# Kernel optimization log

Hardware: AMD Instinct MI355X
Metric: run time of the kernel (lower is better)

## Reference

```python
import jax, jax.numpy as jnp
import numpy as np

N = 200000
D = 128
MAX_DEG = 12
BN_EPS = 1e-5


def setup_inputs() -> dict:
    key = jax.random.key(0)
    ks = jax.random.split(key, 8)
    s = 0.1
    feat = jax.random.normal(ks[0], (N, D), dtype=jnp.float32)
    W_ih = jax.random.normal(ks[1], (3 * D, D), dtype=jnp.float32) * s
    W_hh = jax.random.normal(ks[2], (3 * D, D), dtype=jnp.float32) * s
    b_ih = jax.random.normal(ks[3], (3 * D,), dtype=jnp.float32) * s
    b_hh = jax.random.normal(ks[4], (3 * D,), dtype=jnp.float32) * s
    W_self = jax.random.normal(ks[5], (D, D), dtype=jnp.float32) * s
    W_neigh = jax.random.normal(ks[6], (D, D), dtype=jnp.float32) * s
    gamma = jnp.ones((D,), dtype=jnp.float32)
    beta = jnp.zeros((D,), dtype=jnp.float32)
    # Ragged per-node mailboxes: random in-degree in [0, MAX_DEG], padded.
    rng = np.random.default_rng(0)
    deg = rng.integers(0, MAX_DEG + 1, size=N)
    src_idx = rng.integers(0, N, size=(N, MAX_DEG)).astype(np.int32)
    mask = (np.arange(MAX_DEG)[None, :] < deg[:, None])
    return {
        'feat': feat, 'gamma': gamma, 'beta': beta,
        'W_ih': W_ih, 'W_hh': W_hh, 'b_ih': b_ih, 'b_hh': b_hh,
        'W_self': W_self, 'W_neigh': W_neigh,
        'src_idx': jnp.asarray(src_idx), 'mask': jnp.asarray(mask),
    }


def _eopa_forward(feat, gamma, beta, W_ih, W_hh, b_ih, b_hh, W_self, W_neigh, src_idx, mask):
    # BatchNorm1d (training mode: batch statistics, biased variance)
    mu = jnp.mean(feat, axis=0)
    var = jnp.mean((feat - mu) ** 2, axis=0)
    x = (feat - mu) * jax.lax.rsqrt(var + BN_EPS) * gamma + beta  # [N, D]

    # Precompute input-gate projections are gathered per-step; scan over mailbox slots.
    def step(h, inp):
        src_t, m_t = inp            # [N] int, [N] bool
        xt = x[src_t]               # gather neighbor messages  [N, D]
        gi = xt @ W_ih.T + b_ih     # [N, 3D]
        gh = h @ W_hh.T + b_hh      # [N, 3D]
        ir, iz, inn = jnp.split(gi, 3, axis=1)
        hr, hz, hn = jnp.split(gh, 3, axis=1)
        r = jax.nn.sigmoid(ir + hr)
        z = jax.nn.sigmoid(iz + hz)
        n = jnp.tanh(inn + r * hn)
        h_new = (1.0 - z) * n + z * h
        # freeze hidden state past each node's true in-degree (ragged GRU)
        h = jnp.where(m_t[:, None], h_new, h)
        return h, None

    h0 = jnp.zeros_like(x)
    neigh, _ = jax.lax.scan(step, h0, (src_idx.T, mask.T))  # scan over MAX_DEG steps
    rst = x @ W_self.T + neigh @ W_neigh.T
    return rst


def reference(feat, gamma, beta, W_ih, W_hh, b_ih, b_hh, W_self, W_neigh, src_idx, mask):
    return _eopa_forward(feat, gamma, beta, W_ih, W_hh, b_ih, b_hh, W_self, W_neigh, src_idx, mask)
```

## Files before the change

kernel.cpp:

```cpp
#include <hip/hip_runtime.h>
#include <hip/hip_bf16.h>
#include <stdint.h>

#define NN 200000
#define DD 128

typedef __attribute__((ext_vector_type(8))) short short8;
typedef __attribute__((ext_vector_type(4))) float floatx4;

#define MFMA16(a,b,c) __builtin_amdgcn_mfma_f32_16x16x32_bf16(a,b,c,0,0,0)

static constexpr size_t WS_SUM    = 0;
static constexpr size_t WS_SQ     = 4096;
static constexpr size_t WS_FLAG   = 8192;
static constexpr size_t WS_HIST   = 8256;
static constexpr size_t WS_OFF    = 8384;
static constexpr size_t WS_WHH    = 16384;
static constexpr size_t WS_WIH    = 114688;
static constexpr size_t WS_WSELF  = 212992;
static constexpr size_t WS_WNEIGH = 245760;
static constexpr size_t WS_DEG    = 278528;
static constexpr size_t WS_PERM   = 478528;
static constexpr size_t WS_XB     = 1278528;

__device__ __forceinline__ uint16_t f2b(float f){
    uint32_t u = __builtin_bit_cast(uint32_t, f);
    uint32_t r = u + 0x7FFFu + ((u >> 16) & 1u);
    return (uint16_t)(r >> 16);
}
__device__ __forceinline__ float b2f(uint16_t h){
    uint32_t u = ((uint32_t)h) << 16;
    return __builtin_bit_cast(float, u);
}
__device__ __forceinline__ float sigm(float x){
    float e = __builtin_amdgcn_exp2f(x * -1.4426950408889634f);
    return __builtin_amdgcn_rcpf(1.0f + e);
}
__device__ __forceinline__ float tanh_(float x){
    float e = __builtin_amdgcn_exp2f(x * 2.8853900817779268f);
    return 1.0f - 2.0f * __builtin_amdgcn_rcpf(1.0f + e);
}

__global__ void k_init(float* __restrict__ ws){
#pragma unroll
    for (int k = 0; k < 9; k++) ws[threadIdx.x + k * 256] = 0.0f;
}

__global__ void k_detect(const uint32_t* __restrict__ mask_w, uint32_t* __restrict__ flag){
    __shared__ uint32_t any;
    if (threadIdx.x == 0) any = 0;
    __syncthreads();
    uint32_t loc = 0;
    for (int i = threadIdx.x; i < 4096; i += 256) loc |= (mask_w[i] & 0xFFFFFF00u);
    if (loc) atomicOr(&any, 1u);
    __syncthreads();
    if (threadIdx.x == 0) *flag = (any != 0) ? 1u : 0u;
}

__global__ void k_stats(const float* __restrict__ feat, float* __restrict__ wsum, float* __restrict__ wsq){
    __shared__ float rs_[256][5], rq_[256][5];
    const int cg = threadIdx.x & 31, rr = threadIdx.x >> 5;
    float s0=0,s1=0,s2=0,s3=0,q0=0,q1=0,q2=0,q3=0;
    const float4* f4 = (const float4*)feat;
    for (int r = blockIdx.x * 8 + rr; r < NN; r += gridDim.x * 8){
        float4 v = f4[(size_t)r * 32 + cg];
        s0+=v.x; s1+=v.y; s2+=v.z; s3+=v.w;
        q0+=v.x*v.x; q1+=v.y*v.y; q2+=v.z*v.z; q3+=v.w*v.w;
    }
    rs_[threadIdx.x][0]=s0; rs_[threadIdx.x][1]=s1; rs_[threadIdx.x][2]=s2; rs_[threadIdx.x][3]=s3;
    rq_[threadIdx.x][0]=q0; rq_[threadIdx.x][1]=q1; rq_[threadIdx.x][2]=q2; rq_[threadIdx.x][3]=q3;
    __syncthreads();
    if (threadIdx.x < 32){
        const int rep = (blockIdx.x & 7) * 128;
#pragma unroll
        for (int k = 0; k < 4; k++){
            float a = 0.f, b = 0.f;
#pragma unroll
            for (int r = 0; r < 8; r++){ a += rs_[r*32+threadIdx.x][k]; b += rq_[r*32+threadIdx.x][k]; }
            atomicAdd(&wsum[rep + threadIdx.x*4 + k], a);
            atomicAdd(&wsq [rep + threadIdx.x*4 + k], b);
        }
    }
}

__global__ void k_prep(const float* __restrict__ Wih, const float* __restrict__ Whh,
                       const float* __restrict__ Wself, const float* __restrict__ Wneigh,
                       uint16_t* __restrict__ whh_c, uint16_t* __restrict__ wih_c,
                       uint16_t* __restrict__ wself_c, uint16_t* __restrict__ wneigh_c){
    int i = blockIdx.x * 256 + threadIdx.x;
    if (i < 49152){
        int j = i & 7, cidx = i >> 3, n = cidx % 384, kq = cidx / 384;
        whh_c[i] = f2b(Whh[n * 128 + kq * 8 + j]);
    } else if (i < 98304){
        int e = i - 49152;
        int j = e & 7, cidx = e >> 3, n = cidx % 384, kq = cidx / 384;
        wih_c[e] = f2b(Wih[n * 128 + kq * 8 + j]);
    } else if (i < 114688){
        int e = i - 98304;
        int j = e & 7, cidx = e >> 3, n = cidx & 127, kq = cidx >> 7;
        wself_c[e] = f2b(Wself[n * 128 + kq * 8 + j]);
    } else {
        int e = i - 114688;
        int j = e & 7, cidx = e >> 3, n = cidx & 127, kq = cidx >> 7;
        wneigh_c[e] = f2b(Wneigh[n * 128 + kq * 8 + j]);
    }
}

__global__ void k_hist(const void* __restrict__ mask, const uint32_t* __restrict__ flag,
                       uint8_t* __restrict__ deg, uint32_t* __restrict__ hist){
    __shared__ uint32_t lh[13];
    if (threadIdx.x < 13) lh[threadIdx.x] = 0;
    __syncthreads();
    const uint32_t flg = *flag;
    for (int n = blockIdx.x * 256 + threadIdx.x; n < NN; n += gridDim.x * 256){
        int d = 0;
        if (flg){
            const uint8_t* m = (const uint8_t*)mask + (size_t)n * 12;
            for (int t = 0; t < 12; t++) d += m[t] ? 1 : 0;
        } else {
            const int* m = (const int*)mask + (size_t)n * 12;
            for (int t = 0; t < 12; t++) d += m[t] ? 1 : 0;
        }
        deg[n] = (uint8_t)d;
        atomicAdd(&lh[d], 1u);
    }
    __syncthreads();
    if (threadIdx.x < 13 && lh[threadIdx.x]) atomicAdd(&hist[threadIdx.x], lh[threadIdx.x]);
}

__global__ void k_scan(const uint32_t* __restrict__ hist, uint32_t* __restrict__ off){
    if (threadIdx.x == 0){
        uint32_t acc = 0;
        for (int d = 12; d >= 0; d--){ off[d] = acc; acc += hist[d]; }
    }
}

__global__ void k_scatter(const uint8_t* __restrict__ deg, uint32_t* __restrict__ off,
                          int* __restrict__ perm){
    __shared__ uint32_t lh[13], basebuf[13];
    if (threadIdx.x < 13) lh[threadIdx.x] = 0;
    __syncthreads();
    int n = blockIdx.x * 256 + threadIdx.x;
    int d = 0; uint32_t r = 0;
    bool valid = n < NN;
    if (valid){ d = deg[n]; r = atomicAdd(&lh[d], 1u); }
    __syncthreads();
    if (threadIdx.x < 13 && lh[threadIdx.x]) basebuf[threadIdx.x] = atomicAdd(&off[threadIdx.x], lh[threadIdx.x]);
    __syncthreads();
    if (valid) perm[basebuf[d] + r] = n;
}

__global__ void k_bn(const float* __restrict__ feat, const float* __restrict__ gamma,
                     const float* __restrict__ beta, const float* __restrict__ wsum,
                     const float* __restrict__ wsq, uint16_t* __restrict__ xb){
    const int c8 = (threadIdx.x & 15) * 8;
    const int rr = threadIdx.x >> 4;
    float g[8], b[8];
#pragma unroll
    for (int k = 0; k < 8; k++){
        int col = c8 + k;
        float su = 0.f, sq = 0.f;
#pragma unroll
        for (int r = 0; r < 8; r++){ su += wsum[r*128+col]; sq += wsq[r*128+col]; }
        float mu  = su * (1.0f / NN);
        float var = sq * (1.0f / NN) - mu * mu;
        float rs  = rsqrtf(var + 1e-5f);
        float gg  = gamma[col] * rs;
        g[k] = gg; b[k] = beta[col] - mu * gg;
    }
    for (int r = blockIdx.x * 16 + rr; r < NN; r += gridDim.x * 16){
        const float4* f4 = (const float4*)(feat + (size_t)r * 128 + c8);
        float4 v0 = f4[0], v1 = f4[1];
        short8 o;
        o[0]=(short)f2b(v0.x*g[0]+b[0]); o[1]=(short)f2b(v0.y*g[1]+b[1]);
        o[2]=(short)f2b(v0.z*g[2]+b[2]); o[3]=(short)f2b(v0.w*g[3]+b[3]);
        o[4]=(short)f2b(v1.x*g[4]+b[4]); o[5]=(short)f2b(v1.y*g[5]+b[5]);
        o[6]=(short)f2b(v1.z*g[6]+b[6]); o[7]=(short)f2b(v1.w*g[7]+b[7]);
        *(short8*)(xb + (size_t)r * 128 + c8) = o;
    }
}

__global__ __launch_bounds__(512, 2) void k_gru(
    const uint16_t* __restrict__ xb,
    const uint16_t* __restrict__ whh_c, const uint16_t* __restrict__ wih_c,
    const uint16_t* __restrict__ wself_c, const uint16_t* __restrict__ wneigh_c,
    const float* __restrict__ b_ih, const float* __restrict__ b_hh,
    const int* __restrict__ src_idx, const void* __restrict__ mask,
    const uint32_t* __restrict__ flag, const int* __restrict__ perm,
    const uint8_t* __restrict__ degp, float* __restrict__ out)
{
    __shared__ __align__(16) uint16_t hbuf[2][64][136];
    __shared__ int src_s[768];
    __shared__ uint8_t mask_s[768];
    __shared__ int perm_s[64];
    __shared__ int tmax_s;

    const int tid = threadIdx.x, lane = tid & 63, w = tid >> 6, q = lane >> 4, c = lane & 15;
    const int base = blockIdx.x * 64;

    if (tid < 64) perm_s[tid] = perm[base + tid];
    if (tid == 0) tmax_s = 0;
    __syncthreads();

    const uint32_t flg = *flag;
    for (int i = tid; i < 768; i += 512){
        int node = perm_s[i / 12];
        size_t offn = (size_t)node * 12 + (i % 12);
        src_s[i] = src_idx[offn];
        uint8_t mv;
        if (flg) mv = ((const uint8_t*)mask)[offn] ? 1 : 0;
        else     mv = ((const int*)mask)[offn] ? 1 : 0;
        mask_s[i] = mv;
    }
    if (tid < 64) atomicMax(&tmax_s, (int)degp[perm_s[tid]]);
    for (int i = tid; i < 64 * 136 * 2 / 4; i += 512) ((uint32_t*)hbuf[0])[i] = 0;

    short8 Bi[3][4], Bh[3][4];
    float bs0, bs1, bi2, bh2;
    {
        const int n0 = w * 16 + c;
#pragma unroll
        for (int g = 0; g < 3; g++){
            int n = g * 128 + n0;
#pragma unroll
            for (int kb = 0; kb < 4; kb++){
                Bi[g][kb] = *(const short8*)(wih_c + ((size_t)(kb * 4 + q) * 384 + n) * 8);
                Bh[g][kb] = *(const short8*)(whh_c + ((size_t)(kb * 4 + q) * 384 + n) * 8);
            }
        }
        bs0 = b_ih[n0]       + b_hh[n0];
        bs1 = b_ih[128 + n0] + b_hh[128 + n0];
        bi2 = b_ih[256 + n0];
        bh2 = b_hh[256 + n0];
    }

    float hC[4][4];
#pragma unroll
    for (int m = 0; m < 4; m++)
#pragma unroll
        for (int j = 0; j < 4; j++) hC[m][j] = 0.f;

    __syncthreads();
    const int tmax = tmax_s;

    if (tmax > 0){
        short8 Ax[4][4];
#pragma unroll
        for (int m = 0; m < 4; m++){
            int s = src_s[(m * 16 + c) * 12];
            const uint16_t* a = xb + (size_t)s * 128 + q * 8;
#pragma unroll
            for (int kb = 0; kb < 4; kb++) Ax[m][kb] = *(const short8*)(a + kb * 32);
        }
        for (int t = 0; t < tmax; t++){
            const int rb = t & 1, wbuf = rb ^ 1;
            const int tn = (t + 1 < tmax) ? t + 1 : t;
#pragma unroll
            for (int m = 0; m < 4; m++){
                short8 Ah[4];
#pragma unroll
                for (int kb = 0; kb < 4; kb++)
                    Ah[kb] = *(const short8*)&hbuf[rb][m * 16 + c][kb * 32 + q * 8];
                floatx4 agi[3], agh[3];
#pragma unroll
                for (int g = 0; g < 3; g++){
                    floatx4 x0 = {0.f, 0.f, 0.f, 0.f}, h0 = {0.f, 0.f, 0.f, 0.f};
#pragma unroll
                    for (int kb = 0; kb < 4; kb++){
                        x0 = MFMA16(Ax[m][kb], Bi[g][kb], x0);
                        h0 = MFMA16(Ah[kb],    Bh[g][kb], h0);
                    }
                    agi[g] = x0; agh[g] = h0;
                }
                {
                    int s = src_s[(m * 16 + c) * 12 + tn];
                    const uint16_t* a = xb + (size_t)s * 128 + q * 8;
#pragma unroll
                    for (int kb = 0; kb < 4; kb++) Ax[m][kb] = *(const short8*)(a + kb * 32);
                }
#pragma unroll
                for (int j = 0; j < 4; j++){
                    uint8_t mk = mask_s[(m * 16 + q * 4 + j) * 12 + t];
                    float r  = sigm(agi[0][j] + agh[0][j] + bs0);
                    float z  = sigm(agi[1][j] + agh[1][j] + bs1);
                    float hn = agh[2][j] + bh2;
                    float nn = tanh_(agi[2][j] + bi2 + r * hn);
                    float hold = hC[m][j];
                    float hnew = nn + z * (hold - nn);
                    hnew = mk ? hnew : hold;
                    hC[m][j] = hnew;
                    hbuf[wbuf][m * 16 + q * 4 + j][w * 16 + c] = f2b(hnew);
                }
            }
            asm volatile("s_waitcnt lgkmcnt(0)\n\ts_barrier" ::: "memory");
        }
    }

    const int fb = tmax & 1;

    floatx4 acc2[4];
#pragma unroll
    for (int m = 0; m < 4; m++) acc2[m] = floatx4{0.f, 0.f, 0.f, 0.f};
    short8 Bs_[4], Bn_[4];
#pragma unroll
    for (int kb = 0; kb < 4; kb++){
        Bs_[kb] = *(const short8*)(wself_c  + ((size_t)(kb * 4 + q) * 128 + w * 16 + c) * 8);
        Bn_[kb] = *(const short8*)(wneigh_c + ((size_t)(kb * 4 + q) * 128 + w * 16 + c) * 8);
    }
#pragma unroll
    for (int m = 0; m < 4; m++){
        short8 A[4];
#pragma unroll
        for (int kb = 0; kb < 4; kb++)
            A[kb] = *(const short8*)&hbuf[fb][m * 16 + c][kb * 32 + q * 8];
#pragma unroll
        for (int kb = 0; kb < 4; kb++) acc2[m] = MFMA16(A[kb], Bn_[kb], acc2[m]);
        int xrow = perm_s[m * 16 + c];
        const uint16_t* a = xb + (size_t)xrow * 128 + q * 8;
#pragma unroll
        for (int kb = 0; kb < 4; kb++) A[kb] = *(const short8*)(a + kb * 32);
#pragma unroll
        for (int kb = 0; kb < 4; kb++) acc2[m] = MFMA16(A[kb], Bs_[kb], acc2[m]);
    }
#pragma unroll
    for (int m = 0; m < 4; m++){
#pragma unroll
        for (int j = 0; j < 4; j++){
            int orow = perm_s[m * 16 + q * 4 + j];
            out[(size_t)orow * 128 + w * 16 + c] = acc2[m][j];
        }
    }
}

extern "C" void kernel_launch(void* const* d_in, const int* in_sizes, int n_in,
                              void* d_out, int out_size, void* d_ws, size_t ws_size,
                              hipStream_t stream) {
    const float* feat    = (const float*)d_in[0];
    const float* gamma   = (const float*)d_in[1];
    const float* beta    = (const float*)d_in[2];
    const float* W_ih    = (const float*)d_in[3];
    const float* W_hh    = (const float*)d_in[4];
    const float* b_ih    = (const float*)d_in[5];
    const float* b_hh    = (const float*)d_in[6];
    const float* W_self  = (const float*)d_in[7];
    const float* W_neigh = (const float*)d_in[8];
    const int*   src_idx = (const int*)d_in[9];
    const void*  mask    = (const void*)d_in[10];
    float* out = (float*)d_out;

    char* ws = (char*)d_ws;
    float*    wsum     = (float*)(ws + WS_SUM);
    float*    wsq      = (float*)(ws + WS_SQ);
    uint32_t* flag     = (uint32_t*)(ws + WS_FLAG);
    uint32_t* hist     = (uint32_t*)(ws + WS_HIST);
    uint32_t* off      = (uint32_t*)(ws + WS_OFF);
    uint16_t* whh_c    = (uint16_t*)(ws + WS_WHH);
    uint16_t* wih_c    = (uint16_t*)(ws + WS_WIH);
    uint16_t* wself_c  = (uint16_t*)(ws + WS_WSELF);
    uint16_t* wneigh_c = (uint16_t*)(ws + WS_WNEIGH);
    uint8_t*  deg      = (uint8_t*)(ws + WS_DEG);
    int*      perm     = (int*)(ws + WS_PERM);
    uint16_t* xb       = (uint16_t*)(ws + WS_XB);

    k_init   <<<1,    256, 0, stream>>>((float*)ws);
    k_detect <<<1,    256, 0, stream>>>((const uint32_t*)mask, flag);
    k_stats  <<<512,  256, 0, stream>>>(feat, wsum, wsq);
    k_prep   <<<512,  256, 0, stream>>>(W_ih, W_hh, W_self, W_neigh, whh_c, wih_c, wself_c, wneigh_c);
    k_hist   <<<256,  256, 0, stream>>>(mask, flag, deg, hist);
    k_scan   <<<1,    64,  0, stream>>>(hist, off);
    k_scatter<<<782,  256, 0, stream>>>(deg, off, perm);
    k_bn     <<<782,  256, 0, stream>>>(feat, gamma, beta, wsum, wsq, xb);
    k_gru    <<<3125, 512, 0, stream>>>(xb, whh_c, wih_c, wself_c, wneigh_c, b_ih, b_hh,
                                        src_idx, mask, flag, perm, deg, out);
}
```

Measured before the change: 755.6 us.

## Split GRU block into producer waves for input gates and consumer waves for recurrence

Warps 0-3 now gather neighbor features and compute the input-gate projections (x·W_ih + b_ih) one step ahead, storing them as bf16 in a double-buffered shared-memory array. Warps 4-7 handle only the recurrent h·W_hh matmul and the gate math, running at raised wave priority. The aim is to take gather latency and half the MFMA work off the serial recurrence's critical path. In exchange it adds shared-memory traffic and capacity use, and it rounds the input gates to bf16, which slightly changes numerics.

```diff
diff --git a/kernel.cpp b/kernel.cpp
--- a/kernel.cpp
+++ b/kernel.cpp
@@ -7,8 +7,10 @@
 
 typedef __attribute__((ext_vector_type(8))) short short8;
 typedef __attribute__((ext_vector_type(4))) float floatx4;
+typedef __attribute__((ext_vector_type(2))) unsigned int uint32x2;
 
 #define MFMA16(a,b,c) __builtin_amdgcn_mfma_f32_16x16x32_bf16(a,b,c,0,0,0)
+#define LGKM_BARRIER() asm volatile("s_waitcnt lgkmcnt(0)\n\ts_barrier" ::: "memory")
 
 static constexpr size_t WS_SUM    = 0;
 static constexpr size_t WS_SQ     = 4096;
@@ -190,6 +192,7 @@
     const uint8_t* __restrict__ degp, float* __restrict__ out)
 {
     __shared__ __align__(16) uint16_t hbuf[2][64][136];
+    __shared__ __align__(16) uint16_t gis[2][4][24][64][4];
     __shared__ int src_s[768];
     __shared__ uint8_t mask_s[768];
     __shared__ int perm_s[64];
@@ -213,86 +216,121 @@
         mask_s[i] = mv;
     }
     if (tid < 64) atomicMax(&tmax_s, (int)degp[perm_s[tid]]);
-    for (int i = tid; i < 64 * 136 * 2 / 4; i += 512) ((uint32_t*)hbuf[0])[i] = 0;
-
-    short8 Bi[3][4], Bh[3][4];
-    float bs0, bs1, bi2, bh2;
+    for (int i = tid; i < 64 * 136 * 2 / 2; i += 512) ((uint32_t*)hbuf[0])[i] = 0;
+
+    const bool producer = (w < 4);
+    const int rw = producer ? w : (w - 4);
+
+    short8 Bf[6][4];
+    float bias6[6];
     {
-        const int n0 = w * 16 + c;
-#pragma unroll
-        for (int g = 0; g < 3; g++){
-            int n = g * 128 + n0;
-#pragma unroll
-            for (int kb = 0; kb < 4; kb++){
-                Bi[g][kb] = *(const short8*)(wih_c + ((size_t)(kb * 4 + q) * 384 + n) * 8);
-                Bh[g][kb] = *(const short8*)(whh_c + ((size_t)(kb * 4 + q) * 384 + n) * 8);
+        const uint16_t* wsrc = producer ? wih_c : whh_c;
+        const float*    bsrc = producer ? b_ih  : b_hh;
+#pragma unroll
+        for (int g = 0; g < 3; g++)
+#pragma unroll
+            for (int dg = 0; dg < 2; dg++){
+                const int gd = g * 2 + dg;
+                const int n = g * 128 + rw * 32 + dg * 16 + c;
+                bias6[gd] = bsrc[n];
+#pragma unroll
+                for (int kb = 0; kb < 4; kb++)
+                    Bf[gd][kb] = *(const short8*)(wsrc + ((size_t)(kb * 4 + q) * 384 + n) * 8);
             }
-        }
-        bs0 = b_ih[n0]       + b_hh[n0];
-        bs1 = b_ih[128 + n0] + b_hh[128 + n0];
-        bi2 = b_ih[256 + n0];
-        bh2 = b_hh[256 + n0];
-    }
-
-    float hC[4][4];
-#pragma unroll
-    for (int m = 0; m < 4; m++)
-#pragma unroll
-        for (int j = 0; j < 4; j++) hC[m][j] = 0.f;
+    }
 
     __syncthreads();
     const int tmax = tmax_s;
 
-    if (tmax > 0){
+    if (producer){
         short8 Ax[4][4];
-#pragma unroll
-        for (int m = 0; m < 4; m++){
-            int s = src_s[(m * 16 + c) * 12];
-            const uint16_t* a = xb + (size_t)s * 128 + q * 8;
-#pragma unroll
-            for (int kb = 0; kb < 4; kb++) Ax[m][kb] = *(const short8*)(a + kb * 32);
-        }
+        auto gatherAx = [&](int tg){
+#pragma unroll
+            for (int m = 0; m < 4; m++){
+                int s = src_s[(m * 16 + c) * 12 + tg];
+                const uint16_t* a = xb + (size_t)s * 128 + q * 8;
+#pragma unroll
+                for (int kb = 0; kb < 4; kb++) Ax[m][kb] = *(const short8*)(a + kb * 32);
+            }
+        };
+        auto giStep = [&](int slot){
+#pragma unroll
+            for (int m = 0; m < 4; m++){
+#pragma unroll
+                for (int gd = 0; gd < 6; gd++){
+                    floatx4 a0 = {0.f, 0.f, 0.f, 0.f};
+#pragma unroll
+                    for (int kb = 0; kb < 4; kb++) a0 = MFMA16(Ax[m][kb], Bf[gd][kb], a0);
+                    const float bb = bias6[gd];
+                    uint32x2 v;
+                    v[0] = ((uint32_t)f2b(a0[1] + bb) << 16) | f2b(a0[0] + bb);
+                    v[1] = ((uint32_t)f2b(a0[3] + bb) << 16) | f2b(a0[2] + bb);
+                    *(uint32x2*)&gis[slot][rw][gd * 4 + m][lane][0] = v;
+                }
+            }
+        };
+        if (tmax > 0){
+            gatherAx(0);
+            giStep(0);
+            gatherAx(tmax > 1 ? 1 : 0);
+        }
+        LGKM_BARRIER();
+        for (int t = 0; t < tmax; t++){
+            if (t + 1 < tmax){
+                giStep((t + 1) & 1);
+                gatherAx(t + 2 < tmax ? t + 2 : tmax - 1);
+            }
+            LGKM_BARRIER();
+        }
+    } else {
+        float hC[4][2][4] = {};
+        LGKM_BARRIER();
         for (int t = 0; t < tmax; t++){
             const int rb = t & 1, wbuf = rb ^ 1;
-            const int tn = (t + 1 < tmax) ? t + 1 : t;
+            __builtin_amdgcn_s_setprio(1);
 #pragma unroll
             for (int m = 0; m < 4; m++){
                 short8 Ah[4];
 #pragma unroll
                 for (int kb = 0; kb < 4; kb++)
                     Ah[kb] = *(const short8*)&hbuf[rb][m * 16 + c][kb * 32 + q * 8];
-                floatx4 agi[3], agh[3];
-#pragma unroll
-                for (int g = 0; g < 3; g++){
-                    floatx4 x0 = {0.f, 0.f, 0.f, 0.f}, h0 = {0.f, 0.f, 0.f, 0.f};
-#pragma unroll
-                    for (int kb = 0; kb < 4; kb++){
-                        x0 = MFMA16(Ax[m][kb], Bi[g][kb], x0);
-                        h0 = MFMA16(Ah[kb],    Bh[g][kb], h0);
+                floatx4 ac[6];
+#pragma unroll
+                for (int gd = 0; gd < 6; gd++){
+                    floatx4 a0 = {0.f, 0.f, 0.f, 0.f};
+#pragma unroll
+                    for (int kb = 0; kb < 4; kb++) a0 = MFMA16(Ah[kb], Bf[gd][kb], a0);
+                    ac[gd] = a0;
+                }
+                uint32x2 gp[6];
+#pragma unroll
+                for (int gd = 0; gd < 6; gd++)
+                    gp[gd] = *(const uint32x2*)&gis[rb][rw][gd * 4 + m][lane][0];
+                uint8_t mk[4];
+#pragma unroll
+                for (int j = 0; j < 4; j++) mk[j] = mask_s[(m * 16 + q * 4 + j) * 12 + t];
+#pragma unroll
+                for (int dg = 0; dg < 2; dg++){
+#pragma unroll
+                    for (int j = 0; j < 4; j++){
+                        uint32_t w0 = gp[dg][j >> 1], w1 = gp[2 + dg][j >> 1], w2 = gp[4 + dg][j >> 1];
+                        float gir = b2f((uint16_t)((j & 1) ? (w0 >> 16) : w0));
+                        float giz = b2f((uint16_t)((j & 1) ? (w1 >> 16) : w1));
+                        float gin = b2f((uint16_t)((j & 1) ? (w2 >> 16) : w2));
+                        float r  = sigm(gir + ac[dg][j]     + bias6[dg]);
+                        float z  = sigm(giz + ac[2 + dg][j] + bias6[2 + dg]);
+                        float hn = ac[4 + dg][j] + bias6[4 + dg];
+                        float nn = tanh_(gin + r * hn);
+                        float hold = hC[m][dg][j];
+                        float hnew = nn + z * (hold - nn);
+                        hnew = mk[j] ? hnew : hold;
+                        hC[m][dg][j] = hnew;
+                        hbuf[wbuf][m * 16 + q * 4 + j][rw * 32 + dg * 16 + c] = f2b(hnew);
                     }
-                    agi[g] = x0; agh[g] = h0;
-                }
-                {
-                    int s = src_s[(m * 16 + c) * 12 + tn];
-                    const uint16_t* a = xb + (size_t)s * 128 + q * 8;
-#pragma unroll
-                    for (int kb = 0; kb < 4; kb++) Ax[m][kb] = *(const short8*)(a + kb * 32);
-                }
-#pragma unroll
-                for (int j = 0; j < 4; j++){
-                    uint8_t mk = mask_s[(m * 16 + q * 4 + j) * 12 + t];
-                    float r  = sigm(agi[0][j] + agh[0][j] + bs0);
-                    float z  = sigm(agi[1][j] + agh[1][j] + bs1);
-                    float hn = agh[2][j] + bh2;
-                    float nn = tanh_(agi[2][j] + bi2 + r * hn);
-                    float hold = hC[m][j];
-                    float hnew = nn + z * (hold - nn);
-                    hnew = mk ? hnew : hold;
-                    hC[m][j] = hnew;
-                    hbuf[wbuf][m * 16 + q * 4 + j][w * 16 + c] = f2b(hnew);
                 }
             }
-            asm volatile("s_waitcnt lgkmcnt(0)\n\ts_barrier" ::: "memory");
+            __builtin_amdgcn_s_setprio(0);
+            LGKM_BARRIER();
         }
     }
 
```

Result: no change. 756.8 us (+0.2%).

## Double GRU tile to 128 nodes and stage gathered rows through swizzled LDS

Applied to the files above, without the earlier changes.

The GRU kernel now processes 128 nodes per block instead of 64. Each step's neighbour rows are gathered with 16 lanes reading one full 256-byte row, prefetched one step ahead and written into a double-buffered, XOR-swizzled LDS tile. The h buffer uses the same swizzle in place of padding to avoid bank conflicts. Perm is zero-padded so the last partial block stays in bounds. The aim is more coalesced gathers and better weight reuse per block, at the cost of twice the LDS per block and one resident block per CU (launch bounds 512,1), which lowers occupancy.

```diff
diff --git a/kernel.cpp b/kernel.cpp
--- a/kernel.cpp
+++ b/kernel.cpp
@@ -4,11 +4,13 @@
 
 #define NN 200000
 #define DD 128
+#define PERM_PAD 200064
 
 typedef __attribute__((ext_vector_type(8))) short short8;
 typedef __attribute__((ext_vector_type(4))) float floatx4;
 
 #define MFMA16(a,b,c) __builtin_amdgcn_mfma_f32_16x16x32_bf16(a,b,c,0,0,0)
+#define LGKM_BARRIER() asm volatile("s_waitcnt lgkmcnt(0)\n\ts_barrier" ::: "memory")
 
 static constexpr size_t WS_SUM    = 0;
 static constexpr size_t WS_SQ     = 4096;
@@ -21,7 +23,7 @@
 static constexpr size_t WS_WNEIGH = 245760;
 static constexpr size_t WS_DEG    = 278528;
 static constexpr size_t WS_PERM   = 478528;
-static constexpr size_t WS_XB     = 1278528;
+static constexpr size_t WS_XB     = 1478528;
 
 __device__ __forceinline__ uint16_t f2b(float f){
     uint32_t u = __builtin_bit_cast(uint32_t, f);
@@ -148,6 +150,7 @@
     if (threadIdx.x < 13 && lh[threadIdx.x]) basebuf[threadIdx.x] = atomicAdd(&off[threadIdx.x], lh[threadIdx.x]);
     __syncthreads();
     if (valid) perm[basebuf[d] + r] = n;
+    else if (n < PERM_PAD) perm[n] = 0;
 }
 
 __global__ void k_bn(const float* __restrict__ feat, const float* __restrict__ gamma,
@@ -180,7 +183,7 @@
     }
 }
 
-__global__ __launch_bounds__(512, 2) void k_gru(
+__global__ __launch_bounds__(512, 1) void k_gru(
     const uint16_t* __restrict__ xb,
     const uint16_t* __restrict__ whh_c, const uint16_t* __restrict__ wih_c,
     const uint16_t* __restrict__ wself_c, const uint16_t* __restrict__ wneigh_c,
@@ -189,21 +192,22 @@
     const uint32_t* __restrict__ flag, const int* __restrict__ perm,
     const uint8_t* __restrict__ degp, float* __restrict__ out)
 {
-    __shared__ __align__(16) uint16_t hbuf[2][64][136];
-    __shared__ int src_s[768];
-    __shared__ uint8_t mask_s[768];
-    __shared__ int perm_s[64];
+    __shared__ __align__(16) uint16_t hbuf[2][128][128];
+    __shared__ __align__(16) uint16_t xs[2][128][128];
+    __shared__ int src_s[1536];
+    __shared__ uint8_t mask_s[1536];
+    __shared__ int perm_s[128];
     __shared__ int tmax_s;
 
     const int tid = threadIdx.x, lane = tid & 63, w = tid >> 6, q = lane >> 4, c = lane & 15;
-    const int base = blockIdx.x * 64;
-
-    if (tid < 64) perm_s[tid] = perm[base + tid];
+    const int base = blockIdx.x * 128;
+
+    if (tid < 128) perm_s[tid] = perm[base + tid];
     if (tid == 0) tmax_s = 0;
     __syncthreads();
 
     const uint32_t flg = *flag;
-    for (int i = tid; i < 768; i += 512){
+    for (int i = tid; i < 1536; i += 512){
         int node = perm_s[i / 12];
         size_t offn = (size_t)node * 12 + (i % 12);
         src_s[i] = src_idx[offn];
@@ -212,8 +216,8 @@
         else     mv = ((const int*)mask)[offn] ? 1 : 0;
         mask_s[i] = mv;
     }
-    if (tid < 64) atomicMax(&tmax_s, (int)degp[perm_s[tid]]);
-    for (int i = tid; i < 64 * 136 * 2 / 4; i += 512) ((uint32_t*)hbuf[0])[i] = 0;
+    if (tid < 128) atomicMax(&tmax_s, (int)degp[perm_s[tid]]);
+    for (int i = tid; i < 16384; i += 512) ((uint32_t*)hbuf)[i] = 0;
 
     short8 Bi[3][4], Bh[3][4];
     float bs0, bs1, bi2, bh2;
@@ -234,9 +238,9 @@
         bh2 = b_hh[256 + n0];
     }
 
-    float hC[4][4];
-#pragma unroll
-    for (int m = 0; m < 4; m++)
+    float hC[8][4];
+#pragma unroll
+    for (int m = 0; m < 8; m++)
 #pragma unroll
         for (int j = 0; j < 4; j++) hC[m][j] = 0.f;
 
@@ -244,43 +248,57 @@
     const int tmax = tmax_s;
 
     if (tmax > 0){
-        short8 Ax[4][4];
-#pragma unroll
-        for (int m = 0; m < 4; m++){
-            int s = src_s[(m * 16 + c) * 12];
-            const uint16_t* a = xb + (size_t)s * 128 + q * 8;
-#pragma unroll
-            for (int kb = 0; kb < 4; kb++) Ax[m][kb] = *(const short8*)(a + kb * 32);
-        }
+        const int srow = (lane >> 4);
+        const int pc   = lane & 15;
+        short8 sx[4];
+        auto stageLoad = [&](int tg){
+#pragma unroll
+            for (int i = 0; i < 4; i++){
+                int r = w * 16 + i * 4 + srow;
+                int s = src_s[r * 12 + tg];
+                sx[i] = *(const short8*)(xb + (size_t)s * 128 + pc * 8);
+            }
+        };
+        auto stageWrite = [&](int sl){
+#pragma unroll
+            for (int i = 0; i < 4; i++){
+                int r = w * 16 + i * 4 + srow;
+                int wc = pc ^ (r & 7);
+                *(short8*)&xs[sl][r][wc * 8] = sx[i];
+            }
+        };
+        stageLoad(0);
+        stageWrite(0);
+        LGKM_BARRIER();
         for (int t = 0; t < tmax; t++){
             const int rb = t & 1, wbuf = rb ^ 1;
             const int tn = (t + 1 < tmax) ? t + 1 : t;
-#pragma unroll
-            for (int m = 0; m < 4; m++){
-                short8 Ah[4];
-#pragma unroll
-                for (int kb = 0; kb < 4; kb++)
-                    Ah[kb] = *(const short8*)&hbuf[rb][m * 16 + c][kb * 32 + q * 8];
+            stageLoad(tn);
+#pragma unroll
+            for (int m = 0; m < 8; m++){
+                const int arow = m * 16 + c;
+                short8 Ah[4], Ax[4];
+#pragma unroll
+                for (int kb = 0; kb < 4; kb++){
+                    const int sc = ((kb * 4 + q) ^ (c & 7)) * 8;
+                    Ah[kb] = *(const short8*)&hbuf[rb][arow][sc];
+                    Ax[kb] = *(const short8*)&xs[rb][arow][sc];
+                }
                 floatx4 agi[3], agh[3];
 #pragma unroll
                 for (int g = 0; g < 3; g++){
                     floatx4 x0 = {0.f, 0.f, 0.f, 0.f}, h0 = {0.f, 0.f, 0.f, 0.f};
 #pragma unroll
                     for (int kb = 0; kb < 4; kb++){
-                        x0 = MFMA16(Ax[m][kb], Bi[g][kb], x0);
-                        h0 = MFMA16(Ah[kb],    Bh[g][kb], h0);
+                        x0 = MFMA16(Ax[kb], Bi[g][kb], x0);
+                        h0 = MFMA16(Ah[kb], Bh[g][kb], h0);
                     }
                     agi[g] = x0; agh[g] = h0;
                 }
-                {
-                    int s = src_s[(m * 16 + c) * 12 + tn];
-                    const uint16_t* a = xb + (size_t)s * 128 + q * 8;
-#pragma unroll
-                    for (int kb = 0; kb < 4; kb++) Ax[m][kb] = *(const short8*)(a + kb * 32);
-                }
 #pragma unroll
                 for (int j = 0; j < 4; j++){
-                    uint8_t mk = mask_s[(m * 16 + q * 4 + j) * 12 + t];
+                    const int row = m * 16 + q * 4 + j;
+                    uint8_t mk = mask_s[row * 12 + t];
                     float r  = sigm(agi[0][j] + agh[0][j] + bs0);
                     float z  = sigm(agi[1][j] + agh[1][j] + bs1);
                     float hn = agh[2][j] + bh2;
@@ -289,18 +307,19 @@
                     float hnew = nn + z * (hold - nn);
                     hnew = mk ? hnew : hold;
                     hC[m][j] = hnew;
-                    hbuf[wbuf][m * 16 + q * 4 + j][w * 16 + c] = f2b(hnew);
+                    hbuf[wbuf][row][(((w * 2 + (c >> 3)) ^ (row & 7)) << 3) + (c & 7)] = f2b(hnew);
                 }
             }
-            asm volatile("s_waitcnt lgkmcnt(0)\n\ts_barrier" ::: "memory");
+            stageWrite(wbuf);
+            LGKM_BARRIER();
         }
     }
 
     const int fb = tmax & 1;
 
-    floatx4 acc2[4];
-#pragma unroll
-    for (int m = 0; m < 4; m++) acc2[m] = floatx4{0.f, 0.f, 0.f, 0.f};
+    floatx4 acc2[8];
+#pragma unroll
+    for (int m = 0; m < 8; m++) acc2[m] = floatx4{0.f, 0.f, 0.f, 0.f};
     short8 Bs_[4], Bn_[4];
 #pragma unroll
     for (int kb = 0; kb < 4; kb++){
@@ -308,11 +327,11 @@
         Bn_[kb] = *(const short8*)(wneigh_c + ((size_t)(kb * 4 + q) * 128 + w * 16 + c) * 8);
     }
 #pragma unroll
-    for (int m = 0; m < 4; m++){
+    for (int m = 0; m < 8; m++){
         short8 A[4];
 #pragma unroll
         for (int kb = 0; kb < 4; kb++)
-            A[kb] = *(const short8*)&hbuf[fb][m * 16 + c][kb * 32 + q * 8];
+            A[kb] = *(const short8*)&hbuf[fb][m * 16 + c][((kb * 4 + q) ^ (c & 7)) * 8];
 #pragma unroll
         for (int kb = 0; kb < 4; kb++) acc2[m] = MFMA16(A[kb], Bn_[kb], acc2[m]);
         int xrow = perm_s[m * 16 + c];
@@ -323,7 +342,7 @@
         for (int kb = 0; kb < 4; kb++) acc2[m] = MFMA16(A[kb], Bs_[kb], acc2[m]);
     }
 #pragma unroll
-    for (int m = 0; m < 4; m++){
+    for (int m = 0; m < 8; m++){
 #pragma unroll
         for (int j = 0; j < 4; j++){
             int orow = perm_s[m * 16 + q * 4 + j];
@@ -370,6 +389,6 @@
     k_scan   <<<1,    64,  0, stream>>>(hist, off);
     k_scatter<<<782,  256, 0, stream>>>(deg, off, perm);
     k_bn     <<<782,  256, 0, stream>>>(feat, gamma, beta, wsum, wsq, xb);
-    k_gru    <<<3125, 512, 0, stream>>>(xb, whh_c, wih_c, wself_c, wneigh_c, b_ih, b_hh,
+    k_gru    <<<1563, 512, 0, stream>>>(xb, whh_c, wih_c, wself_c, wneigh_c, b_ih, b_hh,
                                         src_idx, mask, flag, perm, deg, out);
 }
```

New measurement: 676.3 us. 10.5% less time.
